# Optimization experiments

Measured on AMD Instinct MI355X. Metric: run time of the kernel, lower is better.

Reference implementation:

```python
import jax, jax.numpy as jnp
import numpy as np

N_NODES = 50000
N_EDGES = 600000
N_RELS = 500
D = 128


def setup_inputs() -> dict:
    key = jax.random.key(0)
    ks = jax.random.split(key, 8)
    h = jax.random.normal(ks[0], (N_NODES, D), dtype=jnp.float32)
    norm = jax.random.uniform(ks[1], (N_NODES, 1), dtype=jnp.float32)
    rel_emb = jax.random.normal(ks[2], (N_RELS, D), dtype=jnp.float32)
    # xavier-uniform-like scale for square weights
    lim = np.sqrt(6.0 / (D + D)) * np.sqrt(2.0)
    W_neighbor = jax.random.uniform(ks[3], (D, D), dtype=jnp.float32, minval=-lim, maxval=lim)
    loop_weight = jax.random.uniform(ks[4], (D, D), dtype=jnp.float32, minval=-lim, maxval=lim)
    edge_src = jax.random.randint(ks[5], (N_EDGES,), 0, N_NODES, dtype=jnp.int64 if jax.config.jax_enable_x64 else jnp.int32)
    edge_dst = jax.random.randint(ks[6], (N_EDGES,), 0, N_NODES, dtype=edge_src.dtype)
    edge_type = jax.random.randint(ks[7], (N_EDGES,), 0, N_RELS, dtype=edge_src.dtype)
    return {
        "h": h, "norm": norm, "rel_emb": rel_emb,
        "W_neighbor": W_neighbor, "loop_weight": loop_weight,
        "edge_src": edge_src, "edge_dst": edge_dst, "edge_type": edge_type,
    }


def reference(h, norm, rel_emb, W_neighbor, loop_weight, edge_src, edge_dst, edge_type):
    # self-loop message (dense GEMM on node features)
    loop_message = h @ loop_weight  # [N, D]

    # msg_func: gather rel emb + src features, compose ('sub' branch computes node + relation
    # in the original source, reproduced faithfully), dense matmul per edge
    relation = rel_emb[edge_type]          # [E, D] gather
    node = h[edge_src]                     # [E, D] gather
    msg = (node + relation) @ W_neighbor   # [E, D]

    # fn.sum aggregate: scatter-sum messages into destination nodes
    agg = jax.ops.segment_sum(msg, edge_dst, num_segments=h.shape[0])  # [N, D]

    # apply_func: multiply by per-node norm
    node_repr = agg * norm  # [N, D]

    # self_loop add, then activation (relu); dropout=0.0 -> identity
    node_repr = jax.nn.relu(node_repr + loop_message)
    return node_repr
```

## Files before the change

### kernel.cpp

```cpp
#include <hip/hip_runtime.h>

#define NN 50000
#define NE 600000
#define NR 500
#define DD 128
#define CAP 64

#define OFF_CUR  0
#define OFF_BKT  (NN)
#define OFF_HB   (OFF_BKT + NN * CAP)
#define OFF_RELB (OFF_HB + NN * DD / 2)
#define OFF_BP   (OFF_RELB + NR * DD / 2)

typedef __bf16 bf16x8 __attribute__((ext_vector_type(8)));
typedef float  f32x4  __attribute__((ext_vector_type(4)));

#define HB_BLOCKS   3125
#define RELB_BLOCKS 32
#define PB_BLOCKS   128
#define CZ_BLOCKS   196
#define PREP_BLOCKS (HB_BLOCKS + RELB_BLOCKS + PB_BLOCKS + CZ_BLOCKS)

__global__ __launch_bounds__(256) void prep(
    const float* __restrict__ h, const float* __restrict__ rel,
    const float* __restrict__ W, const float* __restrict__ L,
    __bf16* __restrict__ h_bf, __bf16* __restrict__ rel_bf,
    __bf16* __restrict__ Bp, int* __restrict__ cursor)
{
    int b = blockIdx.x;
    if (b < HB_BLOCKS) {
        int t = b * 256 + threadIdx.x;
        const float4* src = (const float4*)h + (size_t)t * 2;
        float4 v0 = src[0], v1 = src[1];
        bf16x8 o;
        o[0]=(__bf16)v0.x; o[1]=(__bf16)v0.y; o[2]=(__bf16)v0.z; o[3]=(__bf16)v0.w;
        o[4]=(__bf16)v1.x; o[5]=(__bf16)v1.y; o[6]=(__bf16)v1.z; o[7]=(__bf16)v1.w;
        *(bf16x8*)(h_bf + (size_t)t * 8) = o;
    } else if (b < HB_BLOCKS + RELB_BLOCKS) {
        int t = (b - HB_BLOCKS) * 256 + threadIdx.x;
        if (t < NR * DD / 8) {
            const float4* src = (const float4*)rel + (size_t)t * 2;
            float4 v0 = src[0], v1 = src[1];
            bf16x8 o;
            o[0]=(__bf16)v0.x; o[1]=(__bf16)v0.y; o[2]=(__bf16)v0.z; o[3]=(__bf16)v0.w;
            o[4]=(__bf16)v1.x; o[5]=(__bf16)v1.y; o[6]=(__bf16)v1.z; o[7]=(__bf16)v1.w;
            *(bf16x8*)(rel_bf + (size_t)t * 8) = o;
        }
    } else if (b < HB_BLOCKS + RELB_BLOCKS + PB_BLOCKS) {
        int t = (b - HB_BLOCKS - RELB_BLOCKS) * 256 + threadIdx.x;
        int lane  = (t >> 3) & 63;
        int ntile = (t >> 9) & 7;
        int kstep = t >> 12;
        int n = ntile * 16 + (lane & 15);
        int k = kstep * 32 + (lane >> 4) * 8 + (t & 7);
        float v = (k < DD) ? W[k * DD + n] : L[(k - DD) * DD + n];
        Bp[t] = (__bf16)v;
    } else {
        int t = (b - HB_BLOCKS - RELB_BLOCKS - PB_BLOCKS) * 256 + threadIdx.x;
        if (t < NN) cursor[t] = 0;
    }
}

__global__ __launch_bounds__(256) void fill_bucket(
    const int* __restrict__ esrc, const int* __restrict__ edst,
    const int* __restrict__ etyp, int* __restrict__ cursor,
    unsigned* __restrict__ bucket)
{
    int e = blockIdx.x * 256 + threadIdx.x;
    if (e < NE) {
        int d = edst[e];
        int pos = atomicAdd(&cursor[d], 1);
        if (pos < CAP)
            bucket[(size_t)d * CAP + pos] = (unsigned)esrc[e] | ((unsigned)etyp[e] << 16);
    }
}

#define AP 264

__global__ __launch_bounds__(256) void fused_gather_mfma(
    const __bf16* __restrict__ h_bf, const __bf16* __restrict__ rel_bf,
    const float* __restrict__ norm, const int* __restrict__ cursor,
    const unsigned* __restrict__ bucket, const __bf16* __restrict__ Bp,
    float* __restrict__ out)
{
    __shared__ __bf16 As[16 * AP];
    int tid = threadIdx.x;
    int row0 = blockIdx.x * 16;
    int g    = tid >> 4;
    int gl   = tid & 15;
    int node = row0 + g;

    int n = cursor[node];
    n = (n < CAP) ? n : CAP;
    const unsigned* bk = bucket + (size_t)node * CAP;
    float acc[8];
#pragma unroll
    for (int j = 0; j < 8; ++j) acc[j] = 0.f;
    int i = 0;
    for (; i + 3 < n; i += 4) {
        unsigned p0 = bk[i], p1 = bk[i+1], p2 = bk[i+2], p3 = bk[i+3];
        bf16x8 a0 = *(const bf16x8*)(h_bf   + (size_t)(p0 & 0xFFFFu) * DD + gl * 8);
        bf16x8 b0 = *(const bf16x8*)(rel_bf + (size_t)(p0 >> 16)     * DD + gl * 8);
        bf16x8 a1 = *(const bf16x8*)(h_bf   + (size_t)(p1 & 0xFFFFu) * DD + gl * 8);
        bf16x8 b1 = *(const bf16x8*)(rel_bf + (size_t)(p1 >> 16)     * DD + gl * 8);
        bf16x8 a2 = *(const bf16x8*)(h_bf   + (size_t)(p2 & 0xFFFFu) * DD + gl * 8);
        bf16x8 b2 = *(const bf16x8*)(rel_bf + (size_t)(p2 >> 16)     * DD + gl * 8);
        bf16x8 a3 = *(const bf16x8*)(h_bf   + (size_t)(p3 & 0xFFFFu) * DD + gl * 8);
        bf16x8 b3 = *(const bf16x8*)(rel_bf + (size_t)(p3 >> 16)     * DD + gl * 8);
#pragma unroll
        for (int j = 0; j < 8; ++j)
            acc[j] += (((float)a0[j] + (float)b0[j]) + ((float)a1[j] + (float)b1[j]))
                    + (((float)a2[j] + (float)b2[j]) + ((float)a3[j] + (float)b3[j]));
    }
    for (; i < n; ++i) {
        unsigned p0 = bk[i];
        bf16x8 a0 = *(const bf16x8*)(h_bf   + (size_t)(p0 & 0xFFFFu) * DD + gl * 8);
        bf16x8 b0 = *(const bf16x8*)(rel_bf + (size_t)(p0 >> 16)     * DD + gl * 8);
#pragma unroll
        for (int j = 0; j < 8; ++j) acc[j] += (float)a0[j] + (float)b0[j];
    }
    float sc = norm[node];
    bf16x8 o;
#pragma unroll
    for (int j = 0; j < 8; ++j) o[j] = (__bf16)(acc[j] * sc);
    *(bf16x8*)&As[g * AP + gl * 8] = o;
    *(bf16x8*)&As[g * AP + DD + gl * 8] =
        *(const bf16x8*)(h_bf + (size_t)node * DD + gl * 8);
    __syncthreads();

    int lane = tid & 63;
    int wave = tid >> 6;
    int aoff = (lane & 15) * AP + (lane >> 4) * 8;

    f32x4 c0 = (f32x4)0.f, c1 = (f32x4)0.f;
    int nt0 = wave * 2;
#pragma unroll
    for (int kstep = 0; kstep < 8; ++kstep) {
        bf16x8 a = *(const bf16x8*)&As[aoff + kstep * 32];
        const __bf16* bbase = Bp + ((size_t)(kstep * 8 + nt0) * 64 + lane) * 8;
        bf16x8 b0 = *(const bf16x8*)bbase;
        bf16x8 b1 = *(const bf16x8*)(bbase + 64 * 8);
        c0 = __builtin_amdgcn_mfma_f32_16x16x32_bf16(a, b0, c0, 0, 0, 0);
        c1 = __builtin_amdgcn_mfma_f32_16x16x32_bf16(a, b1, c1, 0, 0, 0);
    }

    int quad = lane >> 4;
    int col  = lane & 15;
#pragma unroll
    for (int reg = 0; reg < 4; ++reg) {
        float* op = out + (size_t)(row0 + quad * 4 + reg) * DD + col;
        op[nt0 * 16]       = fmaxf(c0[reg], 0.f);
        op[(nt0 + 1) * 16] = fmaxf(c1[reg], 0.f);
    }
}

extern "C" void kernel_launch(void* const* d_in, const int* in_sizes, int n_in,
                              void* d_out, int out_size, void* d_ws, size_t ws_size,
                              hipStream_t stream) {
    const float* h    = (const float*)d_in[0];
    const float* norm = (const float*)d_in[1];
    const float* rel  = (const float*)d_in[2];
    const float* W    = (const float*)d_in[3];
    const float* L    = (const float*)d_in[4];
    const int* esrc   = (const int*)d_in[5];
    const int* edst   = (const int*)d_in[6];
    const int* etyp   = (const int*)d_in[7];
    float* out = (float*)d_out;

    int* ws = (int*)d_ws;
    int* cursor      = ws + OFF_CUR;
    unsigned* bucket = (unsigned*)(ws + OFF_BKT);
    __bf16* h_bf     = (__bf16*)(ws + OFF_HB);
    __bf16* rel_bf   = (__bf16*)(ws + OFF_RELB);
    __bf16* Bp       = (__bf16*)(ws + OFF_BP);

    prep<<<PREP_BLOCKS, 256, 0, stream>>>(h, rel, W, L, h_bf, rel_bf, Bp, cursor);
    fill_bucket<<<(NE + 255) / 256, 256, 0, stream>>>(esrc, edst, etyp, cursor, bucket);
    fused_gather_mfma<<<NN / 16, 256, 0, stream>>>(h_bf, rel_bf, norm, cursor,
                                                   bucket, Bp, out);
}
```

Before: 166.8 us.

## Merge bucket fill into prep kernel and split neighbor gather across two half-groups

Replaces the cursor-zeroing blocks with a memset and folds the edge-bucketing pass into the prep kernel, where each thread handles four edges with vectorized int4 loads. This removes one kernel launch and lets the bucket fill run alongside the bf16 conversions. The gather/MFMA kernel moves to 512 threads: each node's neighbor list is split between two 16-thread halves, and their partial sums are combined through shared memory. Each wave then computes one 16-column MFMA tile instead of two. The aim is more memory-level parallelism in the gather, paid for with an extra barrier, more shared memory and fewer waves resident per CU.

```diff
diff --git a/kernel.cpp b/kernel.cpp
--- a/kernel.cpp
+++ b/kernel.cpp
@@ -15,29 +15,48 @@
 typedef __bf16 bf16x8 __attribute__((ext_vector_type(8)));
 typedef float  f32x4  __attribute__((ext_vector_type(4)));
 
+#define FILL_BLOCKS 586
 #define HB_BLOCKS   3125
 #define RELB_BLOCKS 32
 #define PB_BLOCKS   128
-#define CZ_BLOCKS   196
-#define PREP_BLOCKS (HB_BLOCKS + RELB_BLOCKS + PB_BLOCKS + CZ_BLOCKS)
-
-__global__ __launch_bounds__(256) void prep(
+#define PF_BLOCKS   (FILL_BLOCKS + HB_BLOCKS + RELB_BLOCKS + PB_BLOCKS)
+
+__global__ __launch_bounds__(256) void prep_fill(
     const float* __restrict__ h, const float* __restrict__ rel,
     const float* __restrict__ W, const float* __restrict__ L,
+    const int* __restrict__ esrc, const int* __restrict__ edst,
+    const int* __restrict__ etyp,
     __bf16* __restrict__ h_bf, __bf16* __restrict__ rel_bf,
-    __bf16* __restrict__ Bp, int* __restrict__ cursor)
+    __bf16* __restrict__ Bp, int* __restrict__ cursor,
+    unsigned* __restrict__ bucket)
 {
     int b = blockIdx.x;
-    if (b < HB_BLOCKS) {
-        int t = b * 256 + threadIdx.x;
+    if (b < FILL_BLOCKS) {
+        int e4 = b * 256 + threadIdx.x;
+        if (e4 < NE / 4) {
+            int4 s = ((const int4*)esrc)[e4];
+            int4 d = ((const int4*)edst)[e4];
+            int4 t = ((const int4*)etyp)[e4];
+            int pos;
+            pos = atomicAdd(&cursor[d.x], 1);
+            if (pos < CAP) bucket[(size_t)d.x * CAP + pos] = (unsigned)s.x | ((unsigned)t.x << 16);
+            pos = atomicAdd(&cursor[d.y], 1);
+            if (pos < CAP) bucket[(size_t)d.y * CAP + pos] = (unsigned)s.y | ((unsigned)t.y << 16);
+            pos = atomicAdd(&cursor[d.z], 1);
+            if (pos < CAP) bucket[(size_t)d.z * CAP + pos] = (unsigned)s.z | ((unsigned)t.z << 16);
+            pos = atomicAdd(&cursor[d.w], 1);
+            if (pos < CAP) bucket[(size_t)d.w * CAP + pos] = (unsigned)s.w | ((unsigned)t.w << 16);
+        }
+    } else if (b < FILL_BLOCKS + HB_BLOCKS) {
+        int t = (b - FILL_BLOCKS) * 256 + threadIdx.x;
         const float4* src = (const float4*)h + (size_t)t * 2;
         float4 v0 = src[0], v1 = src[1];
         bf16x8 o;
         o[0]=(__bf16)v0.x; o[1]=(__bf16)v0.y; o[2]=(__bf16)v0.z; o[3]=(__bf16)v0.w;
         o[4]=(__bf16)v1.x; o[5]=(__bf16)v1.y; o[6]=(__bf16)v1.z; o[7]=(__bf16)v1.w;
         *(bf16x8*)(h_bf + (size_t)t * 8) = o;
-    } else if (b < HB_BLOCKS + RELB_BLOCKS) {
-        int t = (b - HB_BLOCKS) * 256 + threadIdx.x;
+    } else if (b < FILL_BLOCKS + HB_BLOCKS + RELB_BLOCKS) {
+        int t = (b - FILL_BLOCKS - HB_BLOCKS) * 256 + threadIdx.x;
         if (t < NR * DD / 8) {
             const float4* src = (const float4*)rel + (size_t)t * 2;
             float4 v0 = src[0], v1 = src[1];
@@ -46,8 +65,8 @@
             o[4]=(__bf16)v1.x; o[5]=(__bf16)v1.y; o[6]=(__bf16)v1.z; o[7]=(__bf16)v1.w;
             *(bf16x8*)(rel_bf + (size_t)t * 8) = o;
         }
-    } else if (b < HB_BLOCKS + RELB_BLOCKS + PB_BLOCKS) {
-        int t = (b - HB_BLOCKS - RELB_BLOCKS) * 256 + threadIdx.x;
+    } else {
+        int t = (b - FILL_BLOCKS - HB_BLOCKS - RELB_BLOCKS) * 256 + threadIdx.x;
         int lane  = (t >> 3) & 63;
         int ntile = (t >> 9) & 7;
         int kstep = t >> 12;
@@ -55,49 +74,46 @@
         int k = kstep * 32 + (lane >> 4) * 8 + (t & 7);
         float v = (k < DD) ? W[k * DD + n] : L[(k - DD) * DD + n];
         Bp[t] = (__bf16)v;
-    } else {
-        int t = (b - HB_BLOCKS - RELB_BLOCKS - PB_BLOCKS) * 256 + threadIdx.x;
-        if (t < NN) cursor[t] = 0;
     }
 }
 
-__global__ __launch_bounds__(256) void fill_bucket(
-    const int* __restrict__ esrc, const int* __restrict__ edst,
-    const int* __restrict__ etyp, int* __restrict__ cursor,
-    unsigned* __restrict__ bucket)
-{
-    int e = blockIdx.x * 256 + threadIdx.x;
-    if (e < NE) {
-        int d = edst[e];
-        int pos = atomicAdd(&cursor[d], 1);
-        if (pos < CAP)
-            bucket[(size_t)d * CAP + pos] = (unsigned)esrc[e] | ((unsigned)etyp[e] << 16);
-    }
-}
-
 #define AP 264
 
-__global__ __launch_bounds__(256) void fused_gather_mfma(
+__global__ __launch_bounds__(512) void fused_gather_mfma(
     const __bf16* __restrict__ h_bf, const __bf16* __restrict__ rel_bf,
     const float* __restrict__ norm, const int* __restrict__ cursor,
     const unsigned* __restrict__ bucket, const __bf16* __restrict__ Bp,
     float* __restrict__ out)
 {
+    __shared__ float  P[16][2][DD];
     __shared__ __bf16 As[16 * AP];
-    int tid = threadIdx.x;
+    int tid  = threadIdx.x;
     int row0 = blockIdx.x * 16;
-    int g    = tid >> 4;
-    int gl   = tid & 15;
+
+    int g   = tid >> 5;
+    int sub = (tid >> 4) & 1;
+    int gl  = tid & 15;
     int node = row0 + g;
 
     int n = cursor[node];
     n = (n < CAP) ? n : CAP;
+    float sc = 0.f;
+    if (tid < 256) sc = norm[row0 + (tid >> 4)];
+    bf16x8 own_h = (bf16x8)(__bf16)0.f;
+    if (tid >= 256)
+        own_h = *(const bf16x8*)(h_bf + (size_t)(row0 + (tid >> 4) - 16) * DD + (tid & 15) * 8);
+
+    int nh  = (n + 1) >> 1;
+    int beg = sub ? nh : 0;
+    int end = sub ? n  : nh;
     const unsigned* bk = bucket + (size_t)node * CAP;
+
     float acc[8];
 #pragma unroll
     for (int j = 0; j < 8; ++j) acc[j] = 0.f;
-    int i = 0;
-    for (; i + 3 < n; i += 4) {
+
+    int i = beg;
+    for (; i + 3 < end; i += 4) {
         unsigned p0 = bk[i], p1 = bk[i+1], p2 = bk[i+2], p3 = bk[i+3];
         bf16x8 a0 = *(const bf16x8*)(h_bf   + (size_t)(p0 & 0xFFFFu) * DD + gl * 8);
         bf16x8 b0 = *(const bf16x8*)(rel_bf + (size_t)(p0 >> 16)     * DD + gl * 8);
@@ -112,45 +128,53 @@
             acc[j] += (((float)a0[j] + (float)b0[j]) + ((float)a1[j] + (float)b1[j]))
                     + (((float)a2[j] + (float)b2[j]) + ((float)a3[j] + (float)b3[j]));
     }
-    for (; i < n; ++i) {
+    for (; i < end; ++i) {
         unsigned p0 = bk[i];
         bf16x8 a0 = *(const bf16x8*)(h_bf   + (size_t)(p0 & 0xFFFFu) * DD + gl * 8);
         bf16x8 b0 = *(const bf16x8*)(rel_bf + (size_t)(p0 >> 16)     * DD + gl * 8);
 #pragma unroll
         for (int j = 0; j < 8; ++j) acc[j] += (float)a0[j] + (float)b0[j];
     }
-    float sc = norm[node];
-    bf16x8 o;
-#pragma unroll
-    for (int j = 0; j < 8; ++j) o[j] = (__bf16)(acc[j] * sc);
-    *(bf16x8*)&As[g * AP + gl * 8] = o;
-    *(bf16x8*)&As[g * AP + DD + gl * 8] =
-        *(const bf16x8*)(h_bf + (size_t)node * DD + gl * 8);
+
+#pragma unroll
+    for (int c = 0; c < 2; ++c) {
+        f32x4 p;
+        p[0] = acc[c*4+0]; p[1] = acc[c*4+1]; p[2] = acc[c*4+2]; p[3] = acc[c*4+3];
+        *(f32x4*)&P[g][sub][gl * 8 + c * 4] = p;
+    }
+    __syncthreads();
+
+    if (tid < 256) {
+        int g2 = tid >> 4, gl2 = tid & 15;
+        bf16x8 o;
+#pragma unroll
+        for (int j = 0; j < 8; ++j)
+            o[j] = (__bf16)((P[g2][0][gl2 * 8 + j] + P[g2][1][gl2 * 8 + j]) * sc);
+        *(bf16x8*)&As[g2 * AP + gl2 * 8] = o;
+    } else {
+        int g2 = (tid >> 4) - 16, gl2 = tid & 15;
+        *(bf16x8*)&As[g2 * AP + DD + gl2 * 8] = own_h;
+    }
     __syncthreads();
 
     int lane = tid & 63;
     int wave = tid >> 6;
     int aoff = (lane & 15) * AP + (lane >> 4) * 8;
 
-    f32x4 c0 = (f32x4)0.f, c1 = (f32x4)0.f;
-    int nt0 = wave * 2;
+    f32x4 c0 = (f32x4)0.f;
 #pragma unroll
     for (int kstep = 0; kstep < 8; ++kstep) {
         bf16x8 a = *(const bf16x8*)&As[aoff + kstep * 32];
-        const __bf16* bbase = Bp + ((size_t)(kstep * 8 + nt0) * 64 + lane) * 8;
-        bf16x8 b0 = *(const bf16x8*)bbase;
-        bf16x8 b1 = *(const bf16x8*)(bbase + 64 * 8);
-        c0 = __builtin_amdgcn_mfma_f32_16x16x32_bf16(a, b0, c0, 0, 0, 0);
-        c1 = __builtin_amdgcn_mfma_f32_16x16x32_bf16(a, b1, c1, 0, 0, 0);
+        bf16x8 b = *(const bf16x8*)(Bp + ((size_t)(kstep * 8 + wave) * 64 + lane) * 8);
+        c0 = __builtin_amdgcn_mfma_f32_16x16x32_bf16(a, b, c0, 0, 0, 0);
     }
 
     int quad = lane >> 4;
     int col  = lane & 15;
 #pragma unroll
     for (int reg = 0; reg < 4; ++reg) {
-        float* op = out + (size_t)(row0 + quad * 4 + reg) * DD + col;
-        op[nt0 * 16]       = fmaxf(c0[reg], 0.f);
-        op[(nt0 + 1) * 16] = fmaxf(c1[reg], 0.f);
+        out[(size_t)(row0 + quad * 4 + reg) * DD + wave * 16 + col] =
+            fmaxf(c0[reg], 0.f);
     }
 }
 
@@ -174,8 +198,9 @@
     __bf16* rel_bf   = (__bf16*)(ws + OFF_RELB);
     __bf16* Bp       = (__bf16*)(ws + OFF_BP);
 
-    prep<<<PREP_BLOCKS, 256, 0, stream>>>(h, rel, W, L, h_bf, rel_bf, Bp, cursor);
-    fill_bucket<<<(NE + 255) / 256, 256, 0, stream>>>(esrc, edst, etyp, cursor, bucket);
-    fused_gather_mfma<<<NN / 16, 256, 0, stream>>>(h_bf, rel_bf, norm, cursor,
+    (void)hipMemsetAsync(cursor, 0, (size_t)NN * sizeof(int), stream);
+    prep_fill<<<PF_BLOCKS, 256, 0, stream>>>(h, rel, W, L, esrc, edst, etyp,
+                                             h_bf, rel_bf, Bp, cursor, bucket);
+    fused_gather_mfma<<<NN / 16, 512, 0, stream>>>(h_bf, rel_bf, norm, cursor,
                                                    bucket, Bp, out);
 }
```

After: 178.1 us. +6.7%, slower.

## Drop bf16 copy of h, gather fp32 directly and fuse bucket fill into prep

Applied to the files above, without the earlier changes.

Removes the pass that converts all of h to bf16, so the gather kernel reads fp32 source rows directly and converts only the node's own row. The bucket-fill step is merged into the prep kernel, with each thread handling four edges through int4 loads. The cursor zeroing moves to a hipMemsetAsync. This cuts one full read and write of h and one kernel launch, but doubles the bytes per gathered neighbour row in the main kernel.

```diff
diff --git a/kernel.cpp b/kernel.cpp
--- a/kernel.cpp
+++ b/kernel.cpp
@@ -8,36 +8,44 @@
 
 #define OFF_CUR  0
 #define OFF_BKT  (NN)
-#define OFF_HB   (OFF_BKT + NN * CAP)
-#define OFF_RELB (OFF_HB + NN * DD / 2)
+#define OFF_RELB (OFF_BKT + NN * CAP)
 #define OFF_BP   (OFF_RELB + NR * DD / 2)
 
 typedef __bf16 bf16x8 __attribute__((ext_vector_type(8)));
 typedef float  f32x4  __attribute__((ext_vector_type(4)));
 
-#define HB_BLOCKS   3125
+#define FILL_BLOCKS 586
 #define RELB_BLOCKS 32
 #define PB_BLOCKS   128
-#define CZ_BLOCKS   196
-#define PREP_BLOCKS (HB_BLOCKS + RELB_BLOCKS + PB_BLOCKS + CZ_BLOCKS)
+#define FP_BLOCKS   (FILL_BLOCKS + RELB_BLOCKS + PB_BLOCKS)
 
-__global__ __launch_bounds__(256) void prep(
-    const float* __restrict__ h, const float* __restrict__ rel,
+__global__ __launch_bounds__(256) void fill_plus(
+    const float* __restrict__ rel,
     const float* __restrict__ W, const float* __restrict__ L,
-    __bf16* __restrict__ h_bf, __bf16* __restrict__ rel_bf,
-    __bf16* __restrict__ Bp, int* __restrict__ cursor)
+    const int* __restrict__ esrc, const int* __restrict__ edst,
+    const int* __restrict__ etyp,
+    __bf16* __restrict__ rel_bf, __bf16* __restrict__ Bp,
+    int* __restrict__ cursor, unsigned* __restrict__ bucket)
 {
     int b = blockIdx.x;
-    if (b < HB_BLOCKS) {
-        int t = b * 256 + threadIdx.x;
-        const float4* src = (const float4*)h + (size_t)t * 2;
-        float4 v0 = src[0], v1 = src[1];
-        bf16x8 o;
-        o[0]=(__bf16)v0.x; o[1]=(__bf16)v0.y; o[2]=(__bf16)v0.z; o[3]=(__bf16)v0.w;
-        o[4]=(__bf16)v1.x; o[5]=(__bf16)v1.y; o[6]=(__bf16)v1.z; o[7]=(__bf16)v1.w;
-        *(bf16x8*)(h_bf + (size_t)t * 8) = o;
-    } else if (b < HB_BLOCKS + RELB_BLOCKS) {
-        int t = (b - HB_BLOCKS) * 256 + threadIdx.x;
+    if (b < FILL_BLOCKS) {
+        int e4 = b * 256 + threadIdx.x;
+        if (e4 < NE / 4) {
+            int4 s = ((const int4*)esrc)[e4];
+            int4 d = ((const int4*)edst)[e4];
+            int4 t = ((const int4*)etyp)[e4];
+            int pos;
+            pos = atomicAdd(&cursor[d.x], 1);
+            if (pos < CAP) bucket[(size_t)d.x * CAP + pos] = (unsigned)s.x | ((unsigned)t.x << 16);
+            pos = atomicAdd(&cursor[d.y], 1);
+            if (pos < CAP) bucket[(size_t)d.y * CAP + pos] = (unsigned)s.y | ((unsigned)t.y << 16);
+            pos = atomicAdd(&cursor[d.z], 1);
+            if (pos < CAP) bucket[(size_t)d.z * CAP + pos] = (unsigned)s.z | ((unsigned)t.z << 16);
+            pos = atomicAdd(&cursor[d.w], 1);
+            if (pos < CAP) bucket[(size_t)d.w * CAP + pos] = (unsigned)s.w | ((unsigned)t.w << 16);
+        }
+    } else if (b < FILL_BLOCKS + RELB_BLOCKS) {
+        int t = (b - FILL_BLOCKS) * 256 + threadIdx.x;
         if (t < NR * DD / 8) {
             const float4* src = (const float4*)rel + (size_t)t * 2;
             float4 v0 = src[0], v1 = src[1];
@@ -46,8 +54,8 @@
             o[4]=(__bf16)v1.x; o[5]=(__bf16)v1.y; o[6]=(__bf16)v1.z; o[7]=(__bf16)v1.w;
             *(bf16x8*)(rel_bf + (size_t)t * 8) = o;
         }
-    } else if (b < HB_BLOCKS + RELB_BLOCKS + PB_BLOCKS) {
-        int t = (b - HB_BLOCKS - RELB_BLOCKS) * 256 + threadIdx.x;
+    } else {
+        int t = (b - FILL_BLOCKS - RELB_BLOCKS) * 256 + threadIdx.x;
         int lane  = (t >> 3) & 63;
         int ntile = (t >> 9) & 7;
         int kstep = t >> 12;
@@ -55,30 +63,13 @@
         int k = kstep * 32 + (lane >> 4) * 8 + (t & 7);
         float v = (k < DD) ? W[k * DD + n] : L[(k - DD) * DD + n];
         Bp[t] = (__bf16)v;
-    } else {
-        int t = (b - HB_BLOCKS - RELB_BLOCKS - PB_BLOCKS) * 256 + threadIdx.x;
-        if (t < NN) cursor[t] = 0;
-    }
-}
-
-__global__ __launch_bounds__(256) void fill_bucket(
-    const int* __restrict__ esrc, const int* __restrict__ edst,
-    const int* __restrict__ etyp, int* __restrict__ cursor,
-    unsigned* __restrict__ bucket)
-{
-    int e = blockIdx.x * 256 + threadIdx.x;
-    if (e < NE) {
-        int d = edst[e];
-        int pos = atomicAdd(&cursor[d], 1);
-        if (pos < CAP)
-            bucket[(size_t)d * CAP + pos] = (unsigned)esrc[e] | ((unsigned)etyp[e] << 16);
     }
 }
 
 #define AP 264
 
 __global__ __launch_bounds__(256) void fused_gather_mfma(
-    const __bf16* __restrict__ h_bf, const __bf16* __restrict__ rel_bf,
+    const float* __restrict__ h, const __bf16* __restrict__ rel_bf,
     const float* __restrict__ norm, const int* __restrict__ cursor,
     const unsigned* __restrict__ bucket, const __bf16* __restrict__ Bp,
     float* __restrict__ out)
@@ -90,42 +81,63 @@
     int gl   = tid & 15;
     int node = row0 + g;
 
+    const float4* ownp = (const float4*)(h + (size_t)node * DD) + gl * 2;
+    float4 ow0 = ownp[0], ow1 = ownp[1];
+    float sc = norm[node];
     int n = cursor[node];
     n = (n < CAP) ? n : CAP;
     const unsigned* bk = bucket + (size_t)node * CAP;
+
     float acc[8];
 #pragma unroll
     for (int j = 0; j < 8; ++j) acc[j] = 0.f;
+
     int i = 0;
     for (; i + 3 < n; i += 4) {
         unsigned p0 = bk[i], p1 = bk[i+1], p2 = bk[i+2], p3 = bk[i+3];
-        bf16x8 a0 = *(const bf16x8*)(h_bf   + (size_t)(p0 & 0xFFFFu) * DD + gl * 8);
-        bf16x8 b0 = *(const bf16x8*)(rel_bf + (size_t)(p0 >> 16)     * DD + gl * 8);
-        bf16x8 a1 = *(const bf16x8*)(h_bf   + (size_t)(p1 & 0xFFFFu) * DD + gl * 8);
-        bf16x8 b1 = *(const bf16x8*)(rel_bf + (size_t)(p1 >> 16)     * DD + gl * 8);
-        bf16x8 a2 = *(const bf16x8*)(h_bf   + (size_t)(p2 & 0xFFFFu) * DD + gl * 8);
-        bf16x8 b2 = *(const bf16x8*)(rel_bf + (size_t)(p2 >> 16)     * DD + gl * 8);
-        bf16x8 a3 = *(const bf16x8*)(h_bf   + (size_t)(p3 & 0xFFFFu) * DD + gl * 8);
-        bf16x8 b3 = *(const bf16x8*)(rel_bf + (size_t)(p3 >> 16)     * DD + gl * 8);
+        const float4* h0 = (const float4*)(h + (size_t)(p0 & 0xFFFFu) * DD) + gl * 2;
+        const float4* h1 = (const float4*)(h + (size_t)(p1 & 0xFFFFu) * DD) + gl * 2;
+        const float4* h2 = (const float4*)(h + (size_t)(p2 & 0xFFFFu) * DD) + gl * 2;
+        const float4* h3 = (const float4*)(h + (size_t)(p3 & 0xFFFFu) * DD) + gl * 2;
+        float4 x00 = h0[0], x01 = h0[1];
+        float4 x10 = h1[0], x11 = h1[1];
+        float4 x20 = h2[0], x21 = h2[1];
+        float4 x30 = h3[0], x31 = h3[1];
+        bf16x8 r0 = *(const bf16x8*)(rel_bf + (size_t)(p0 >> 16) * DD + gl * 8);
+        bf16x8 r1 = *(const bf16x8*)(rel_bf + (size_t)(p1 >> 16) * DD + gl * 8);
+        bf16x8 r2 = *(const bf16x8*)(rel_bf + (size_t)(p2 >> 16) * DD + gl * 8);
+        bf16x8 r3 = *(const bf16x8*)(rel_bf + (size_t)(p3 >> 16) * DD + gl * 8);
+        acc[0] += (x00.x + x10.x) + (x20.x + x30.x);
+        acc[1] += (x00.y + x10.y) + (x20.y + x30.y);
+        acc[2] += (x00.z + x10.z) + (x20.z + x30.z);
+        acc[3] += (x00.w + x10.w) + (x20.w + x30.w);
+        acc[4] += (x01.x + x11.x) + (x21.x + x31.x);
+        acc[5] += (x01.y + x11.y) + (x21.y + x31.y);
+        acc[6] += (x01.z + x11.z) + (x21.z + x31.z);
+        acc[7] += (x01.w + x11.w) + (x21.w + x31.w);
 #pragma unroll
         for (int j = 0; j < 8; ++j)
-            acc[j] += (((float)a0[j] + (float)b0[j]) + ((float)a1[j] + (float)b1[j]))
-                    + (((float)a2[j] + (float)b2[j]) + ((float)a3[j] + (float)b3[j]));
+            acc[j] += ((float)r0[j] + (float)r1[j]) + ((float)r2[j] + (float)r3[j]);
     }
     for (; i < n; ++i) {
         unsigned p0 = bk[i];
-        bf16x8 a0 = *(const bf16x8*)(h_bf   + (size_t)(p0 & 0xFFFFu) * DD + gl * 8);
-        bf16x8 b0 = *(const bf16x8*)(rel_bf + (size_t)(p0 >> 16)     * DD + gl * 8);
+        const float4* h0 = (const float4*)(h + (size_t)(p0 & 0xFFFFu) * DD) + gl * 2;
+        float4 x00 = h0[0], x01 = h0[1];
+        bf16x8 r0 = *(const bf16x8*)(rel_bf + (size_t)(p0 >> 16) * DD + gl * 8);
+        acc[0] += x00.x; acc[1] += x00.y; acc[2] += x00.z; acc[3] += x00.w;
+        acc[4] += x01.x; acc[5] += x01.y; acc[6] += x01.z; acc[7] += x01.w;
 #pragma unroll
-        for (int j = 0; j < 8; ++j) acc[j] += (float)a0[j] + (float)b0[j];
+        for (int j = 0; j < 8; ++j) acc[j] += (float)r0[j];
     }
-    float sc = norm[node];
+
     bf16x8 o;
 #pragma unroll
     for (int j = 0; j < 8; ++j) o[j] = (__bf16)(acc[j] * sc);
     *(bf16x8*)&As[g * AP + gl * 8] = o;
-    *(bf16x8*)&As[g * AP + DD + gl * 8] =
-        *(const bf16x8*)(h_bf + (size_t)node * DD + gl * 8);
+    bf16x8 oh;
+    oh[0]=(__bf16)ow0.x; oh[1]=(__bf16)ow0.y; oh[2]=(__bf16)ow0.z; oh[3]=(__bf16)ow0.w;
+    oh[4]=(__bf16)ow1.x; oh[5]=(__bf16)ow1.y; oh[6]=(__bf16)ow1.z; oh[7]=(__bf16)ow1.w;
+    *(bf16x8*)&As[g * AP + DD + gl * 8] = oh;
     __syncthreads();
 
     int lane = tid & 63;
@@ -170,12 +182,12 @@
     int* ws = (int*)d_ws;
     int* cursor      = ws + OFF_CUR;
     unsigned* bucket = (unsigned*)(ws + OFF_BKT);
-    __bf16* h_bf     = (__bf16*)(ws + OFF_HB);
     __bf16* rel_bf   = (__bf16*)(ws + OFF_RELB);
     __bf16* Bp       = (__bf16*)(ws + OFF_BP);
 
-    prep<<<PREP_BLOCKS, 256, 0, stream>>>(h, rel, W, L, h_bf, rel_bf, Bp, cursor);
-    fill_bucket<<<(NE + 255) / 256, 256, 0, stream>>>(esrc, edst, etyp, cursor, bucket);
-    fused_gather_mfma<<<NN / 16, 256, 0, stream>>>(h_bf, rel_bf, norm, cursor,
+    (void)hipMemsetAsync(cursor, 0, (size_t)NN * sizeof(int), stream);
+    fill_plus<<<FP_BLOCKS, 256, 0, stream>>>(rel, W, L, esrc, edst, etyp,
+                                             rel_bf, Bp, cursor, bucket);
+    fused_gather_mfma<<<NN / 16, 256, 0, stream>>>(h, rel_bf, norm, cursor,
                                                    bucket, Bp, out);
 }
```

Result: slower. 172.9 us (+3.7%).
